# Performance work log

Measured on AMD Instinct MI355X. Metric: run time of the kernel, lower is better.

The kernel has to match this reference:

```python
import jax, jax.numpy as jnp
import numpy as np
import math

D, H, S, B, E, FF = 768, 12, 1024, 2, 32768, 4 * 768
HD = D // H


def layer_norm(x, g, b, eps=1e-5):
    m = jnp.mean(x, axis=-1, keepdims=True)
    v = jnp.mean((x - m) ** 2, axis=-1, keepdims=True)
    return (x - m) / jnp.sqrt(v + eps) * g + b


def setup_inputs() -> dict:
    key = jax.random.key(0)
    ks = jax.random.split(key, 24)
    w = lambda k, shape: jax.random.normal(k, shape, dtype=jnp.float32) * 0.02
    inp = {
        "x": jax.random.normal(ks[0], (B, S, D), dtype=jnp.float32),
        "adj_mask": jax.random.randint(ks[1], (B, S, S), 0, 2).astype(bool),
        "edge_attr": jax.random.normal(ks[2], (E,), dtype=jnp.float32),
        "edge_index": jax.random.randint(ks[3], (2, E), 0, S),
        "norm1_g": jnp.ones((D,), jnp.float32),
        "norm1_b": jnp.zeros((D,), jnp.float32),
        "Wq": w(ks[4], (D, D)), "bq": jnp.zeros((D,), jnp.float32),
        "Wk": w(ks[5], (D, D)), "bk": jnp.zeros((D,), jnp.float32),
        "Wv": w(ks[6], (D, D)), "bv": jnp.zeros((D,), jnp.float32),
        "Wo": w(ks[7], (D, D)), "bo": jnp.zeros((D,), jnp.float32),
        "norm2_g": jnp.ones((D,), jnp.float32),
        "norm2_b": jnp.zeros((D,), jnp.float32),
        "mlp_W1": w(ks[8], (D, FF)), "mlp_b1": jnp.zeros((FF,), jnp.float32),
        "mlp_W2": w(ks[9], (FF, D)), "mlp_b2": jnp.zeros((D,), jnp.float32),
        # per-head edge-attr MLP: Linear(1,16) -> GELU -> Linear(16,1), stacked over H heads
        "ep_W1": w(ks[10], (H, 16)), "ep_b1": jnp.zeros((H, 16), jnp.float32),
        "ep_W2": w(ks[11], (H, 16)), "ep_b2": jnp.zeros((H,), jnp.float32),
    }
    return inp


def reference(x, adj_mask, edge_attr, edge_index,
              norm1_g, norm1_b, Wq, bq, Wk, bk, Wv, bv, Wo, bo,
              norm2_g, norm2_b, mlp_W1, mlp_b1, mlp_W2, mlp_b2,
              ep_W1, ep_b1, ep_W2, ep_b2):
    Bb, Ss, Dd = x.shape
    Hh = ep_W1.shape[0]
    hd = Dd // Hh
    residual = x
    nx = layer_norm(x, norm1_g, norm1_b)
    q = (nx @ Wq + bq).reshape(Bb, Ss, Hh, hd).transpose(0, 2, 1, 3)  # [B,H,S,hd]
    k = (nx @ Wk + bk).reshape(Bb, Ss, Hh, hd).transpose(0, 2, 1, 3)
    v = (nx @ Wv + bv).reshape(Bb, Ss, Hh, hd).transpose(0, 2, 1, 3)
    scores = jnp.einsum('bhqd,bhkd->bhqk', q, k) / math.sqrt(hd)
    mask = adj_mask.astype(bool)[:, None]  # [B,1,S,S]
    scores = jnp.where(mask, scores, jnp.float32(-1e9))
    # per-edge per-head bias (computed under no_grad in the original -> stop_gradient)
    h1 = jax.nn.gelu(edge_attr[:, None, None] * ep_W1[None] + ep_b1[None], approximate=False)  # [E,H,16]
    proj = jnp.einsum('ehk,hk->eh', h1, ep_W2) + ep_b2  # [E,H]
    proj = jax.lax.stop_gradient(proj)
    src, dst = edge_index[0], edge_index[1]
    bias = jnp.zeros((Hh, Ss, Ss), x.dtype).at[:, src, dst].set(proj.T)  # [H,S,S]
    scores = scores + jnp.where(mask, bias[None], jnp.float32(0.0))
    attn = jax.nn.softmax(scores, axis=-1)
    out = jnp.einsum('bhqk,bhkd->bhqd', attn, v)
    out = out.transpose(0, 2, 1, 3).reshape(Bb, Ss, Dd)
    x = residual + (out @ Wo + bo)
    y = layer_norm(x, norm2_g, norm2_b)
    y = jax.nn.gelu(y @ mlp_W1 + mlp_b1, approximate=False) @ mlp_W2 + mlp_b2
    return x + y
```

## Files before the change

### kernel.cpp

```cpp
#include <hip/hip_runtime.h>
#include <hip/hip_bf16.h>

#define B_ 2
#define S_ 1024
#define D_ 768
#define H_ 12
#define HD_ 64
#define FF_ 3072
#define E_ 32768
#define QS_ 2304
#define NSPLIT 4
#define NSPLIT_W2 4
#define BHS (B_ * H_ * S_)

typedef short bf16x8 __attribute__((ext_vector_type(8)));
typedef float f32x4 __attribute__((ext_vector_type(4)));

#define SW(row, seg) ((((seg) ^ ((row) & 7)) * 8))

__device__ __forceinline__ unsigned short f2bf(float f) {
    __hip_bfloat16 h = __float2bfloat16(f);
    return __builtin_bit_cast(unsigned short, h);
}
__device__ __forceinline__ float bf2f(unsigned short u) {
    unsigned int v = ((unsigned int)u) << 16;
    return __builtin_bit_cast(float, v);
}
__device__ __forceinline__ float gelu_exact(float x) {
    return 0.5f * x * (1.0f + erff(x * 0.70710678118654752f));
}
__device__ __forceinline__ void gload_lds16(const unsigned short* g, unsigned short* l) {
    __builtin_amdgcn_global_load_lds((const __attribute__((address_space(1))) void*)g,
                                     (__attribute__((address_space(3))) void*)l, 16, 0, 0);
}

__global__ __launch_bounds__(256) void prep_kernel(
    const void* __restrict__ adj, unsigned int* __restrict__ mp, int* __restrict__ winner,
    const float* __restrict__ Wq, const float* __restrict__ Wk, const float* __restrict__ Wv,
    const float* __restrict__ Wo, const float* __restrict__ W1, const float* __restrict__ W2,
    unsigned short* __restrict__ wqkvt, unsigned short* __restrict__ wot,
    unsigned short* __restrict__ w1t, unsigned short* __restrict__ w2t,
    const float* __restrict__ bq, const float* __restrict__ bk, const float* __restrict__ bv,
    float* __restrict__ bqkv,
    const float* __restrict__ x, const float* __restrict__ g1, const float* __restrict__ bn1,
    unsigned short* __restrict__ nxb)
{
    __shared__ float tile[32][33];
    __shared__ unsigned int words[32];
    __shared__ int u8f;
    __shared__ float red[8];
    const int blk = blockIdx.x;
    const int t = threadIdx.x;

    if (blk < 2048) {
        const int b = blk >> 10, q = blk & 1023;
        if (b == 0) {
            int4 v; v.x = -1; v.y = -1; v.z = -1; v.w = -1;
            reinterpret_cast<int4*>(winner)[q * 256 + t] = v;
        }
        if (t < 32) words[t] = 0;
        if (t == 0) u8f = 0;
        __syncthreads();
        const unsigned int* row8 = (const unsigned int*)((const unsigned char*)adj + ((size_t)b * S_ + q) * S_);
        const unsigned int* row32 = (const unsigned int*)((const int*)adj + ((size_t)b * S_ + q) * S_);
        const unsigned int v = row8[t];
        if (v & 0xFF00FF00u) atomicOr(&u8f, 1);
        __syncthreads();
        if (u8f) {
            unsigned int nib = 0;
            if (v & 0x000000FFu) nib |= 1u;
            if (v & 0x0000FF00u) nib |= 2u;
            if (v & 0x00FF0000u) nib |= 4u;
            if (v & 0xFF000000u) nib |= 8u;
            if (nib) atomicOr(&words[t >> 3], nib << ((t & 7) * 4));
        } else {
            for (int i = 0; i < 4; i++) {
                const int k = i * 256 + t;
                if (row32[k]) atomicOr(&words[k >> 5], 1u << (k & 31));
            }
        }
        __syncthreads();
        if (t < 32) mp[((size_t)b * S_ + q) * 32 + t] = words[t];
    } else if (blk < 8960) {
        const int w = blk - 2048;
        const float* src; unsigned short* dst; int K, N, nb, kb;
        if (w < 2304) {
            const int z = w / 576, r = w - z * 576;
            K = 768; N = 768; kb = (r / 24) * 32; nb = (r % 24) * 32;
            src = (z == 0) ? Wq : (z == 1) ? Wk : (z == 2) ? Wv : Wo;
            dst = (z == 3) ? wot : wqkvt + (size_t)z * 768 * 768;
        } else if (w < 4608) {
            const int r = w - 2304;
            K = 768; N = 3072; nb = (r % 96) * 32; kb = (r / 96) * 32;
            src = W1; dst = w1t;
        } else {
            const int r = w - 4608;
            K = 3072; N = 768; kb = (r % 96) * 32; nb = (r / 96) * 32;
            src = W2; dst = w2t;
        }
        const int tx = t & 31, ty = t >> 5;
        for (int r = 0; r < 32; r += 8)
            tile[ty + r][tx] = src[(size_t)(kb + ty + r) * N + nb + tx];
        __syncthreads();
        for (int r = 0; r < 32; r += 8)
            dst[(size_t)(nb + ty + r) * K + kb + tx] = f2bf(tile[tx][ty + r]);
        if (w == 0) {
            for (int i = t; i < QS_; i += 256)
                bqkv[i] = (i < 768) ? bq[i] : (i < 1536) ? bk[i - 768] : bv[i - 1536];
        }
    } else {
        const int row = blk - 8960;
        const float* xr = x + (size_t)row * D_;
        float v0 = xr[t], v1 = xr[t + 256], v2 = xr[t + 512];
        float s = v0 + v1 + v2, s2 = v0 * v0 + v1 * v1 + v2 * v2;
        for (int m = 32; m; m >>= 1) { s += __shfl_xor(s, m); s2 += __shfl_xor(s2, m); }
        const int w = t >> 6;
        if ((t & 63) == 0) { red[w] = s; red[4 + w] = s2; }
        __syncthreads();
        s = red[0] + red[1] + red[2] + red[3];
        s2 = red[4] + red[5] + red[6] + red[7];
        const float mean = s * (1.f / D_);
        const float var = s2 * (1.f / D_) - mean * mean;
        const float rstd = rsqrtf(var + 1e-5f);
        unsigned short* orow = nxb + (size_t)row * D_;
        orow[t]       = f2bf((v0 - mean) * rstd * g1[t]       + bn1[t]);
        orow[t + 256] = f2bf((v1 - mean) * rstd * g1[t + 256] + bn1[t + 256]);
        orow[t + 512] = f2bf((v2 - mean) * rstd * g1[t + 512] + bn1[t + 512]);
    }
}

__global__ __launch_bounds__(256) void ln_kernel(
    const float* __restrict__ x, const float* __restrict__ g,
    const float* __restrict__ b, unsigned short* __restrict__ out)
{
    const int row = blockIdx.x;
    const int t = threadIdx.x;
    const float* xr = x + (size_t)row * D_;
    float v0 = xr[t], v1 = xr[t + 256], v2 = xr[t + 512];
    float s = v0 + v1 + v2, s2 = v0 * v0 + v1 * v1 + v2 * v2;
    for (int m = 32; m; m >>= 1) { s += __shfl_xor(s, m); s2 += __shfl_xor(s2, m); }
    __shared__ float red[8];
    const int w = t >> 6;
    if ((t & 63) == 0) { red[w] = s; red[4 + w] = s2; }
    __syncthreads();
    s = red[0] + red[1] + red[2] + red[3];
    s2 = red[4] + red[5] + red[6] + red[7];
    const float mean = s * (1.f / D_);
    const float var = s2 * (1.f / D_) - mean * mean;
    const float rstd = rsqrtf(var + 1e-5f);
    unsigned short* orow = out + (size_t)row * D_;
    orow[t]       = f2bf((v0 - mean) * rstd * g[t]       + b[t]);
    orow[t + 256] = f2bf((v1 - mean) * rstd * g[t + 256] + b[t + 256]);
    orow[t + 512] = f2bf((v2 - mean) * rstd * g[t + 512] + b[t + 512]);
}

__global__ __launch_bounds__(256) void edge_proj_scatter_kernel(
    const float* __restrict__ ea, const float* __restrict__ W1, const float* __restrict__ b1,
    const float* __restrict__ W2, const float* __restrict__ b2,
    const int* __restrict__ ei, float* __restrict__ proj, int* __restrict__ winner)
{
    const int tid = blockIdx.x * 256 + threadIdx.x;
    const int e = tid / H_, h = tid - e * H_;
    const float a = ea[e];
    float s = 0.f;
    for (int j = 0; j < 16; j++) {
        const float tv = a * W1[h * 16 + j] + b1[h * 16 + j];
        s += gelu_exact(tv) * W2[h * 16 + j];
    }
    proj[tid] = s + b2[h];
    if (h == 0) {
        const int sn = ei[e], dn = ei[E_ + e];
        atomicMax(&winner[sn * S_ + dn], e);
    }
}

__global__ __launch_bounds__(256) void qkv_kernel(
    const unsigned short* __restrict__ A, const unsigned short* __restrict__ Bt,
    const float* __restrict__ bias, unsigned short* __restrict__ qkv,
    unsigned short* __restrict__ vt,
    const int* __restrict__ winner, const float* __restrict__ proj,
    unsigned short* __restrict__ ebias)
{
    const int blk = blockIdx.x;
    const int t = threadIdx.x;
    if (blk >= 288) {
        const int q = blk - 288;
        const int k4 = t * 4;
        const int4 wv = *reinterpret_cast<const int4*>(&winner[q * S_ + k4]);
        for (int h = 0; h < H_; h++) {
            unsigned int lo = 0, hi = 0;
            if (wv.x >= 0) lo |= (unsigned int)f2bf(proj[(size_t)wv.x * H_ + h]);
            if (wv.y >= 0) lo |= ((unsigned int)f2bf(proj[(size_t)wv.y * H_ + h])) << 16;
            if (wv.z >= 0) hi |= (unsigned int)f2bf(proj[(size_t)wv.z * H_ + h]);
            if (wv.w >= 0) hi |= ((unsigned int)f2bf(proj[(size_t)wv.w * H_ + h])) << 16;
            uint2 val; val.x = lo; val.y = hi;
            *reinterpret_cast<uint2*>(&ebias[((size_t)h * S_ + q) * S_ + k4]) = val;
        }
        return;
    }
    __shared__ unsigned short As[128][64];
    __shared__ unsigned short Bs[128][64];
    const int bx = blk % 18, by = blk / 18;
    const int m0 = by * 128, n0 = bx * 128;
    const int w = t >> 6, l = t & 63;
    const int wm = w >> 1, wn = w & 1;
    const int lr = l & 15, g = l >> 4;
    const int lrow8 = l >> 3;
    const int lseg = (l & 7) ^ lrow8;
    f32x4 acc[4][4] = {};
    for (int k0 = 0; k0 < D_; k0 += 64) {
        __syncthreads();
        for (int j = 0; j < 4; j++) {
            const int q = w * 4 + j;
            const int row = q * 8 + lrow8;
            gload_lds16(A  + (size_t)(m0 + row) * D_ + k0 + lseg * 8, &As[q * 8][0]);
            gload_lds16(Bt + (size_t)(n0 + row) * D_ + k0 + lseg * 8, &Bs[q * 8][0]);
        }
        __syncthreads();
        for (int kk = 0; kk < 2; kk++) {
            bf16x8 af[4], bfr[4];
            for (int m = 0; m < 4; m++) {
                const int r = wm * 64 + m * 16 + lr;
                af[m] = *reinterpret_cast<const bf16x8*>(&As[r][SW(r, kk * 4 + g)]);
            }
            for (int n = 0; n < 4; n++) {
                const int r = wn * 64 + n * 16 + lr;
                bfr[n] = *reinterpret_cast<const bf16x8*>(&Bs[r][SW(r, kk * 4 + g)]);
            }
            for (int m = 0; m < 4; m++)
                for (int n = 0; n < 4; n++)
                    acc[m][n] = __builtin_amdgcn_mfma_f32_16x16x32_bf16(af[m], bfr[n], acc[m][n], 0, 0, 0);
        }
    }
    if (n0 >= 1536) {
        for (int m = 0; m < 4; m++)
            for (int n = 0; n < 4; n++) {
                const int col = n0 + wn * 64 + n * 16 + lr;
                const int vcol = col - 1536;
                const int hh = vcol >> 6, d = vcol & 63;
                const float bvv = bias[col];
                const int grow = m0 + wm * 64 + m * 16 + g * 4;
                const int bb = grow >> 10, s = grow & 1023;
                ushort4 o;
                o.x = f2bf(acc[m][n][0] + bvv);
                o.y = f2bf(acc[m][n][1] + bvv);
                o.z = f2bf(acc[m][n][2] + bvv);
                o.w = f2bf(acc[m][n][3] + bvv);
                *reinterpret_cast<ushort4*>(&vt[(((size_t)(bb * H_ + hh) * HD_) + d) * S_ + s]) = o;
            }
    } else {
        for (int m = 0; m < 4; m++)
            for (int n = 0; n < 4; n++) {
                const int col = n0 + wn * 64 + n * 16 + lr;
                const float scl = (col < 768) ? 0.125f : 1.0f;
                const float bvv = bias[col];
                for (int j = 0; j < 4; j++) {
                    const int row = m0 + wm * 64 + m * 16 + g * 4 + j;
                    qkv[(size_t)row * QS_ + col] = f2bf((acc[m][n][j] + bvv) * scl);
                }
            }
    }
}

template<bool RES, bool OUTBF>
__global__ __launch_bounds__(256) void gemm_kernel(
    const unsigned short* __restrict__ A, const unsigned short* __restrict__ Bt,
    const float* __restrict__ bias, const float* __restrict__ res,
    void* __restrict__ outp, int M, int N, int K)
{
    __shared__ unsigned short As[64][40];
    __shared__ unsigned short Bs[64][40];
    const int m0 = blockIdx.y * 64, n0 = blockIdx.x * 64;
    const int t = threadIdx.x;
    const int w = t >> 6, l = t & 63;
    const int wm = w >> 1, wn = w & 1;
    const int r = l & 15, g = l >> 4;
    const int srow = t >> 2, sseg = t & 3;
    f32x4 acc[2][2] = {};
    for (int k0 = 0; k0 < K; k0 += 32) {
        __syncthreads();
        const uint4 av = *reinterpret_cast<const uint4*>(A + (size_t)(m0 + srow) * K + k0 + sseg * 8);
        *reinterpret_cast<uint4*>(&As[srow][sseg * 8]) = av;
        const uint4 bv = *reinterpret_cast<const uint4*>(Bt + (size_t)(n0 + srow) * K + k0 + sseg * 8);
        *reinterpret_cast<uint4*>(&Bs[srow][sseg * 8]) = bv;
        __syncthreads();
        bf16x8 af[2], bfr[2];
        af[0]  = *reinterpret_cast<const bf16x8*>(&As[wm * 32 + r][g * 8]);
        af[1]  = *reinterpret_cast<const bf16x8*>(&As[wm * 32 + 16 + r][g * 8]);
        bfr[0] = *reinterpret_cast<const bf16x8*>(&Bs[wn * 32 + r][g * 8]);
        bfr[1] = *reinterpret_cast<const bf16x8*>(&Bs[wn * 32 + 16 + r][g * 8]);
        for (int m = 0; m < 2; m++)
            for (int n = 0; n < 2; n++)
                acc[m][n] = __builtin_amdgcn_mfma_f32_16x16x32_bf16(af[m], bfr[n], acc[m][n], 0, 0, 0);
    }
    for (int m = 0; m < 2; m++)
        for (int n = 0; n < 2; n++) {
            const int col = n0 + wn * 32 + n * 16 + r;
            const float bvv = bias[col];
            for (int j = 0; j < 4; j++) {
                const int row = m0 + wm * 32 + m * 16 + g * 4 + j;
                float v = acc[m][n][j] + bvv;
                if (RES) v += res[(size_t)row * N + col];
                if (OUTBF) ((unsigned short*)outp)[(size_t)row * N + col] = f2bf(v);
                else       ((float*)outp)[(size_t)row * N + col] = v;
            }
        }
}

template<bool GELU, bool OUTBF, bool SPLITK>
__global__ __launch_bounds__(256) void gemm128_kernel(
    const unsigned short* __restrict__ A, const unsigned short* __restrict__ Bt,
    const float* __restrict__ bias, void* __restrict__ outp,
    int M, int N, int K, int klen, int scale_below)
{
    __shared__ unsigned short As[128][64];
    __shared__ unsigned short Bs[128][64];
    const int m0 = blockIdx.y * 128, n0 = blockIdx.x * 128;
    const int t = threadIdx.x;
    const int w = t >> 6, l = t & 63;
    const int wm = w >> 1, wn = w & 1;
    const int lr = l & 15, g = l >> 4;
    const int lrow8 = l >> 3;
    const int lseg = (l & 7) ^ lrow8;
    const int kbeg = SPLITK ? blockIdx.z * klen : 0;
    const int kend = SPLITK ? kbeg + klen : K;
    f32x4 acc[4][4] = {};
    for (int k0 = kbeg; k0 < kend; k0 += 64) {
        __syncthreads();
        for (int j = 0; j < 4; j++) {
            const int q = w * 4 + j;
            const int row = q * 8 + lrow8;
            gload_lds16(A  + (size_t)(m0 + row) * K + k0 + lseg * 8, &As[q * 8][0]);
            gload_lds16(Bt + (size_t)(n0 + row) * K + k0 + lseg * 8, &Bs[q * 8][0]);
        }
        __syncthreads();
        for (int kk = 0; kk < 2; kk++) {
            bf16x8 af[4], bfr[4];
            for (int m = 0; m < 4; m++) {
                const int r = wm * 64 + m * 16 + lr;
                af[m] = *reinterpret_cast<const bf16x8*>(&As[r][SW(r, kk * 4 + g)]);
            }
            for (int n = 0; n < 4; n++) {
                const int r = wn * 64 + n * 16 + lr;
                bfr[n] = *reinterpret_cast<const bf16x8*>(&Bs[r][SW(r, kk * 4 + g)]);
            }
            for (int m = 0; m < 4; m++)
                for (int n = 0; n < 4; n++)
                    acc[m][n] = __builtin_amdgcn_mfma_f32_16x16x32_bf16(af[m], bfr[n], acc[m][n], 0, 0, 0);
        }
    }
    if (SPLITK) {
        for (int m = 0; m < 4; m++)
            for (int n = 0; n < 4; n++) {
                const int col = n0 + wn * 64 + n * 16 + lr;
                for (int j = 0; j < 4; j++) {
                    const int row = m0 + wm * 64 + m * 16 + g * 4 + j;
                    if (OUTBF) ((unsigned short*)outp)[((size_t)blockIdx.z * M + row) * N + col] = f2bf(acc[m][n][j]);
                    else       ((float*)outp)[((size_t)blockIdx.z * M + row) * N + col] = acc[m][n][j];
                }
            }
    } else {
        for (int m = 0; m < 4; m++)
            for (int n = 0; n < 4; n++) {
                const int col = n0 + wn * 64 + n * 16 + lr;
                const float scl = (col < scale_below) ? 0.125f : 1.0f;
                const float bvv = bias[col];
                for (int j = 0; j < 4; j++) {
                    const int row = m0 + wm * 64 + m * 16 + g * 4 + j;
                    float v = (acc[m][n][j] + bvv) * scl;
                    if (GELU) v = gelu_exact(v);
                    if (OUTBF) ((unsigned short*)outp)[(size_t)row * N + col] = f2bf(v);
                    else       ((float*)outp)[(size_t)row * N + col] = v;
                }
            }
    }
}

__global__ __launch_bounds__(256) void w2_reduce_kernel(
    const unsigned short* __restrict__ part, const float* __restrict__ x2,
    const float* __restrict__ b2, float* __restrict__ out)
{
    const int idx = (blockIdx.x * 256 + threadIdx.x) * 4;
    const int col = idx % D_;
    const float4 xr = *reinterpret_cast<const float4*>(&x2[idx]);
    const float4 bb = *reinterpret_cast<const float4*>(&b2[col]);
    float4 o;
    o.x = xr.x + bb.x; o.y = xr.y + bb.y; o.z = xr.z + bb.z; o.w = xr.w + bb.w;
    for (int s = 0; s < NSPLIT_W2; s++) {
        const uint2 p = *reinterpret_cast<const uint2*>(&part[(size_t)s * B_ * S_ * D_ + idx]);
        o.x += bf2f((unsigned short)(p.x & 0xFFFF));
        o.y += bf2f((unsigned short)(p.x >> 16));
        o.z += bf2f((unsigned short)(p.y & 0xFFFF));
        o.w += bf2f((unsigned short)(p.y >> 16));
    }
    *reinterpret_cast<float4*>(&out[idx]) = o;
}

__global__ __launch_bounds__(256) void attn_mfma_kernel(
    const unsigned short* __restrict__ qkv,
    const unsigned short* __restrict__ vt,
    const unsigned short* __restrict__ ebias,
    const unsigned int* __restrict__ mp,
    unsigned short* __restrict__ pacc,
    float2* __restrict__ pml)
{
    __shared__ unsigned short Ks[64][64];
    __shared__ unsigned short Vs[64][64];
    __shared__ unsigned short Eb[64][72];
    __shared__ unsigned int   Mw[64][2];
    __shared__ unsigned short Ps[4][16][64];
    const int t = threadIdx.x;
    const int w = t >> 6, l = t & 63;
    const int lr = l & 15, g = l >> 4;
    const int qt = blockIdx.x & 15, sp = blockIdx.x >> 4;
    const int q0 = qt * 64;
    const int h = blockIdx.y, b = blockIdx.z;
    const int bh = b * H_ + h;
    const size_t qbase = (size_t)b * S_ * QS_ + h * HD_;
    const size_t kbase = qbase + 768;
    const size_t vtbase = (size_t)bh * HD_ * S_;

    const int qrow = q0 + w * 16 + lr;
    const bf16x8 af0 = *reinterpret_cast<const bf16x8*>(qkv + qbase + (size_t)qrow * QS_ + g * 8);
    const bf16x8 af1 = *reinterpret_cast<const bf16x8*>(qkv + qbase + (size_t)qrow * QS_ + 32 + g * 8);

    float m_run[4], l_run[4];
    f32x4 acc[4] = {};
    for (int j = 0; j < 4; j++) { m_run[j] = -3.0e38f; l_run[j] = 0.f; }

    const int srow = t >> 2, sseg = t & 3;
    const int kt_beg = sp * (S_ / NSPLIT), kt_end = kt_beg + S_ / NSPLIT;

    uint4 kr0, kr1, vr0, vr1, er0, er1;
    unsigned int mr = 0;
    auto load_tile = [&](int kt) {
        const unsigned short* ksrc = qkv + kbase + (size_t)(kt + srow) * QS_ + sseg * 16;
        kr0 = *reinterpret_cast<const uint4*>(ksrc);
        kr1 = *reinterpret_cast<const uint4*>(ksrc + 8);
        const unsigned short* vsrc = vt + vtbase + (size_t)srow * S_ + kt + sseg * 16;
        vr0 = *reinterpret_cast<const uint4*>(vsrc);
        vr1 = *reinterpret_cast<const uint4*>(vsrc + 8);
        const unsigned short* esrc = ebias + ((size_t)h * S_ + q0 + srow) * S_ + kt + sseg * 16;
        er0 = *reinterpret_cast<const uint4*>(esrc);
        er1 = *reinterpret_cast<const uint4*>(esrc + 8);
        if (t < 128) mr = mp[((size_t)b * S_ + q0 + (t >> 1)) * 32 + (kt >> 5) + (t & 1)];
    };
    load_tile(kt_beg);

    for (int kt = kt_beg; kt < kt_end; kt += 64) {
        __syncthreads();
        {
            *reinterpret_cast<uint4*>(&Ks[srow][SW(srow, sseg * 2)])     = kr0;
            *reinterpret_cast<uint4*>(&Ks[srow][SW(srow, sseg * 2 + 1)]) = kr1;
            *reinterpret_cast<uint4*>(&Vs[srow][SW(srow, sseg * 2)])     = vr0;
            *reinterpret_cast<uint4*>(&Vs[srow][SW(srow, sseg * 2 + 1)]) = vr1;
            *reinterpret_cast<uint4*>(&Eb[srow][sseg * 16])     = er0;
            *reinterpret_cast<uint4*>(&Eb[srow][sseg * 16 + 8]) = er1;
            if (t < 128) Mw[t >> 1][t & 1] = mr;
        }
        __syncthreads();
        if (kt + 64 < kt_end) load_tile(kt + 64);
        f32x4 sc[4];
        for (int n = 0; n < 4; n++) {
            const int r = n * 16 + lr;
            const bf16x8 b0 = *reinterpret_cast<const bf16x8*>(&Ks[r][SW(r, g)]);
            const bf16x8 b1 = *reinterpret_cast<const bf16x8*>(&Ks[r][SW(r, 4 + g)]);
            f32x4 z = {};
            z = __builtin_amdgcn_mfma_f32_16x16x32_bf16(af0, b0, z, 0, 0, 0);
            z = __builtin_amdgcn_mfma_f32_16x16x32_bf16(af1, b1, z, 0, 0, 0);
            sc[n] = z;
        }
        float tmax[4] = {-3.0e38f, -3.0e38f, -3.0e38f, -3.0e38f};
        for (int n = 0; n < 4; n++) {
            for (int j = 0; j < 4; j++) {
                const int rq = w * 16 + g * 4 + j;
                const unsigned int word = Mw[rq][n >> 1];
                const bool msk = (word >> ((n & 1) * 16 + lr)) & 1;
                float sval;
                if (msk) sval = sc[n][j] + bf2f(Eb[rq][n * 16 + lr]);
                else sval = -1e9f;
                sc[n][j] = sval;
                tmax[j] = fmaxf(tmax[j], sval);
            }
        }
        float pscale[4];
        for (int j = 0; j < 4; j++) {
            float tm = tmax[j];
            tm = fmaxf(tm, __shfl_xor(tm, 1));
            tm = fmaxf(tm, __shfl_xor(tm, 2));
            tm = fmaxf(tm, __shfl_xor(tm, 4));
            tm = fmaxf(tm, __shfl_xor(tm, 8));
            const float mnew = fmaxf(m_run[j], tm);
            pscale[j] = __expf(m_run[j] - mnew);
            m_run[j] = mnew;
            l_run[j] *= pscale[j];
        }
        float psum[4] = {0.f, 0.f, 0.f, 0.f};
        for (int n = 0; n < 4; n++) {
            for (int j = 0; j < 4; j++) {
                const float p = __expf(sc[n][j] - m_run[j]);
                psum[j] += p;
                const int row = g * 4 + j;
                Ps[w][row][SW(row, n * 2 + (lr >> 3)) + (lr & 7)] = f2bf(p);
            }
        }
        for (int j = 0; j < 4; j++) {
            float s = psum[j];
            s += __shfl_xor(s, 1); s += __shfl_xor(s, 2);
            s += __shfl_xor(s, 4); s += __shfl_xor(s, 8);
            l_run[j] += s;
            for (int n2 = 0; n2 < 4; n2++) acc[n2][j] *= pscale[j];
        }
        const bf16x8 pa0 = *reinterpret_cast<const bf16x8*>(&Ps[w][lr][SW(lr, g)]);
        const bf16x8 pa1 = *reinterpret_cast<const bf16x8*>(&Ps[w][lr][SW(lr, 4 + g)]);
        for (int n2 = 0; n2 < 4; n2++) {
            const int r = n2 * 16 + lr;
            const bf16x8 vb0 = *reinterpret_cast<const bf16x8*>(&Vs[r][SW(r, g)]);
            const bf16x8 vb1 = *reinterpret_cast<const bf16x8*>(&Vs[r][SW(r, 4 + g)]);
            acc[n2] = __builtin_amdgcn_mfma_f32_16x16x32_bf16(pa0, vb0, acc[n2], 0, 0, 0);
            acc[n2] = __builtin_amdgcn_mfma_f32_16x16x32_bf16(pa1, vb1, acc[n2], 0, 0, 0);
        }
    }
    const size_t prow = (size_t)sp * BHS + (size_t)bh * S_;
    for (int j = 0; j < 4; j++) {
        const int qg = q0 + w * 16 + g * 4 + j;
        for (int n2 = 0; n2 < 4; n2++)
            pacc[(prow + qg) * 64 + n2 * 16 + lr] = f2bf(acc[n2][j]);
        if (lr == 0) { float2 v; v.x = m_run[j]; v.y = l_run[j]; pml[prow + qg] = v; }
    }
}

__global__ __launch_bounds__(256) void attn_combine_kernel(
    const unsigned short* __restrict__ pacc, const float2* __restrict__ pml,
    unsigned short* __restrict__ attnb)
{
    const int idx = (blockIdx.x * 256 + threadIdx.x) * 4;
    const int r = idx >> 6, d = idx & 63;
    float2 ml[NSPLIT];
    float mx = -3.0e38f;
    for (int s = 0; s < NSPLIT; s++) {
        ml[s] = pml[(size_t)s * BHS + r];
        mx = fmaxf(mx, ml[s].x);
    }
    float wgt[NSPLIT], L = 0.f;
    for (int s = 0; s < NSPLIT; s++) {
        wgt[s] = __expf(ml[s].x - mx);
        L += ml[s].y * wgt[s];
    }
    const float inv = (L > 0.f) ? 1.f / L : 0.f;
    float4 o = {0.f, 0.f, 0.f, 0.f};
    for (int s = 0; s < NSPLIT; s++) {
        const uint2 p = *reinterpret_cast<const uint2*>(&pacc[((size_t)s * BHS + r) * 64 + d]);
        o.x += bf2f((unsigned short)(p.x & 0xFFFF)) * wgt[s];
        o.y += bf2f((unsigned short)(p.x >> 16)) * wgt[s];
        o.z += bf2f((unsigned short)(p.y & 0xFFFF)) * wgt[s];
        o.w += bf2f((unsigned short)(p.y >> 16)) * wgt[s];
    }
    const int bh = r >> 10, q = r & 1023;
    const int b = bh / H_, h = bh - b * H_;
    ushort4 ov;
    ov.x = f2bf(o.x * inv); ov.y = f2bf(o.y * inv);
    ov.z = f2bf(o.z * inv); ov.w = f2bf(o.w * inv);
    *reinterpret_cast<ushort4*>(&attnb[((size_t)(b * S_ + q)) * D_ + h * HD_ + d]) = ov;
}

extern "C" void kernel_launch(void* const* d_in, const int* in_sizes, int n_in,
                              void* d_out, int out_size, void* d_ws, size_t ws_size,
                              hipStream_t stream)
{
    const float* x    = (const float*)d_in[0];
    const void*  adj  = d_in[1];
    const float* ea   = (const float*)d_in[2];
    const int*   ei   = (const int*)d_in[3];
    const float* g1   = (const float*)d_in[4];
    const float* bn1  = (const float*)d_in[5];
    const float* Wq   = (const float*)d_in[6];
    const float* bq   = (const float*)d_in[7];
    const float* Wk   = (const float*)d_in[8];
    const float* bk   = (const float*)d_in[9];
    const float* Wv   = (const float*)d_in[10];
    const float* bv   = (const float*)d_in[11];
    const float* Wo   = (const float*)d_in[12];
    const float* bo   = (const float*)d_in[13];
    const float* g2   = (const float*)d_in[14];
    const float* bn2  = (const float*)d_in[15];
    const float* W1   = (const float*)d_in[16];
    const float* mb1  = (const float*)d_in[17];
    const float* W2   = (const float*)d_in[18];
    const float* mb2  = (const float*)d_in[19];
    const float* epW1 = (const float*)d_in[20];
    const float* epb1 = (const float*)d_in[21];
    const float* epW2 = (const float*)d_in[22];
    const float* epb2 = (const float*)d_in[23];

    char* ws = (char*)d_ws;
    size_t off = 0;
    auto carve = [&](size_t bytes) -> void* {
        void* p = ws + off;
        off += (bytes + 255) & ~(size_t)255;
        return p;
    };
    unsigned short* wqkvt = (unsigned short*)carve((size_t)QS_ * D_ * 2);
    unsigned short* wot   = (unsigned short*)carve((size_t)D_ * D_ * 2);
    unsigned short* w1t   = (unsigned short*)carve((size_t)FF_ * D_ * 2);
    unsigned short* w2t   = (unsigned short*)carve((size_t)D_ * FF_ * 2);
    float*          bqkv  = (float*)carve((size_t)QS_ * 4);
    float*          proj  = (float*)carve((size_t)E_ * H_ * 4);
    int*            winner= (int*)carve((size_t)S_ * S_ * 4);
    unsigned short* ebias = (unsigned short*)carve((size_t)H_ * S_ * S_ * 2);
    unsigned int*   mpk   = (unsigned int*)carve((size_t)B_ * S_ * 32 * 4);
    unsigned short* nxb   = (unsigned short*)carve((size_t)B_ * S_ * D_ * 2);
    unsigned short* attnb = (unsigned short*)carve((size_t)B_ * S_ * D_ * 2);
    unsigned short* qkv   = (unsigned short*)carve((size_t)B_ * S_ * QS_ * 2);
    unsigned short* vtb   = (unsigned short*)carve((size_t)B_ * S_ * D_ * 2);
    float*          x2f   = (float*)carve((size_t)B_ * S_ * D_ * 4);
    unsigned short* pacc  = (unsigned short*)carve((size_t)NSPLIT * BHS * 64 * 2);
    float2*         pml   = (float2*)carve((size_t)NSPLIT * BHS * 8);
    unsigned short* ln2b = nxb;
    unsigned short* hb   = qkv;
    unsigned short* pw2  = (unsigned short*)ebias;

    const int M = B_ * S_;

    prep_kernel<<<11008, 256, 0, stream>>>(
        adj, mpk, winner,
        Wq, Wk, Wv, Wo, W1, W2, wqkvt, wot, w1t, w2t, bq, bk, bv, bqkv,
        x, g1, bn1, nxb);

    edge_proj_scatter_kernel<<<(E_ * H_) / 256, 256, 0, stream>>>(
        ea, epW1, epb1, epW2, epb2, ei, proj, winner);

    qkv_kernel<<<288 + S_, 256, 0, stream>>>(
        nxb, wqkvt, bqkv, qkv, vtb, winner, proj, ebias);

    attn_mfma_kernel<<<dim3(16 * NSPLIT, H_, B_), 256, 0, stream>>>(
        qkv, vtb, ebias, mpk, pacc, pml);
    attn_combine_kernel<<<(BHS * 64) / 1024, 256, 0, stream>>>(pacc, pml, attnb);

    gemm_kernel<true, false><<<dim3(D_ / 64, M / 64), 256, 0, stream>>>(
        attnb, wot, bo, x, x2f, M, D_, D_);

    ln_kernel<<<M, 256, 0, stream>>>(x2f, g2, bn2, ln2b);

    gemm128_kernel<true, true, false><<<dim3(FF_ / 128, M / 128), 256, 0, stream>>>(
        ln2b, w1t, mb1, hb, M, FF_, D_, D_, 0);
    gemm128_kernel<false, true, true><<<dim3(D_ / 128, M / 128, NSPLIT_W2), 256, 0, stream>>>(
        hb, w2t, mb2, pw2, M, D_, FF_, FF_ / NSPLIT_W2, 0);
    w2_reduce_kernel<<<(M * D_) / 1024, 256, 0, stream>>>(pw2, x2f, mb2, (float*)d_out);
}
```

Baseline: 183.8 us.

## Split-K the Wo projection, fuse its reduction into LN2, fold edge MLP into prep

The Wo GEMM becomes a 2-way split-K kernel that writes bf16 partials, and the residual add, bias and partial reduction move into the LayerNorm-2 kernel, which also writes x2f. The per-edge MLP projection moves into the prep kernel as extra blocks, leaving only a small atomic scatter kernel. The split-K doubles the block count of the small 768x768 GEMM to improve occupancy, and the prep merge removes a separate launch. The cost is extra partial-buffer traffic and bf16 rounding of the partial sums before the residual add.

```diff
diff --git a/kernel.cpp b/kernel.cpp
--- a/kernel.cpp
+++ b/kernel.cpp
@@ -43,7 +43,9 @@
     const float* __restrict__ bq, const float* __restrict__ bk, const float* __restrict__ bv,
     float* __restrict__ bqkv,
     const float* __restrict__ x, const float* __restrict__ g1, const float* __restrict__ bn1,
-    unsigned short* __restrict__ nxb)
+    unsigned short* __restrict__ nxb,
+    const float* __restrict__ ea, const float* __restrict__ epW1, const float* __restrict__ epb1,
+    const float* __restrict__ epW2, const float* __restrict__ epb2, float* __restrict__ proj)
 {
     __shared__ float tile[32][33];
     __shared__ unsigned int words[32];
@@ -108,7 +110,7 @@
             for (int i = t; i < QS_; i += 256)
                 bqkv[i] = (i < 768) ? bq[i] : (i < 1536) ? bk[i - 768] : bv[i - 1536];
         }
-    } else {
+    } else if (blk < 11008) {
         const int row = blk - 8960;
         const float* xr = x + (size_t)row * D_;
         float v0 = xr[t], v1 = xr[t + 256], v2 = xr[t + 512];
@@ -126,17 +128,171 @@
         orow[t]       = f2bf((v0 - mean) * rstd * g1[t]       + bn1[t]);
         orow[t + 256] = f2bf((v1 - mean) * rstd * g1[t + 256] + bn1[t + 256]);
         orow[t + 512] = f2bf((v2 - mean) * rstd * g1[t + 512] + bn1[t + 512]);
-    }
-}
-
-__global__ __launch_bounds__(256) void ln_kernel(
-    const float* __restrict__ x, const float* __restrict__ g,
-    const float* __restrict__ b, unsigned short* __restrict__ out)
+    } else {
+        const int tid = (blk - 11008) * 256 + t;
+        const int e = tid / H_, h = tid - e * H_;
+        const float a = ea[e];
+        float s = 0.f;
+        for (int j = 0; j < 16; j++) {
+            const float tv = a * epW1[h * 16 + j] + epb1[h * 16 + j];
+            s += gelu_exact(tv) * epW2[h * 16 + j];
+        }
+        proj[tid] = s + epb2[h];
+    }
+}
+
+__global__ __launch_bounds__(256) void scatter_kernel(
+    const int* __restrict__ ei, int* __restrict__ winner)
+{
+    const int e = blockIdx.x * 256 + threadIdx.x;
+    const int sn = ei[e], dn = ei[E_ + e];
+    atomicMax(&winner[sn * S_ + dn], e);
+}
+
+__global__ __launch_bounds__(256) void qkv_kernel(
+    const unsigned short* __restrict__ A, const unsigned short* __restrict__ Bt,
+    const float* __restrict__ bias, unsigned short* __restrict__ qkv,
+    unsigned short* __restrict__ vt,
+    const int* __restrict__ winner, const float* __restrict__ proj,
+    unsigned short* __restrict__ ebias)
+{
+    const int blk = blockIdx.x;
+    const int t = threadIdx.x;
+    if (blk >= 288) {
+        const int q = blk - 288;
+        const int k4 = t * 4;
+        const int4 wv = *reinterpret_cast<const int4*>(&winner[q * S_ + k4]);
+        for (int h = 0; h < H_; h++) {
+            unsigned int lo = 0, hi = 0;
+            if (wv.x >= 0) lo |= (unsigned int)f2bf(proj[(size_t)wv.x * H_ + h]);
+            if (wv.y >= 0) lo |= ((unsigned int)f2bf(proj[(size_t)wv.y * H_ + h])) << 16;
+            if (wv.z >= 0) hi |= (unsigned int)f2bf(proj[(size_t)wv.z * H_ + h]);
+            if (wv.w >= 0) hi |= ((unsigned int)f2bf(proj[(size_t)wv.w * H_ + h])) << 16;
+            uint2 val; val.x = lo; val.y = hi;
+            *reinterpret_cast<uint2*>(&ebias[((size_t)h * S_ + q) * S_ + k4]) = val;
+        }
+        return;
+    }
+    __shared__ unsigned short As[128][64];
+    __shared__ unsigned short Bs[128][64];
+    const int bx = blk % 18, by = blk / 18;
+    const int m0 = by * 128, n0 = bx * 128;
+    const int w = t >> 6, l = t & 63;
+    const int wm = w >> 1, wn = w & 1;
+    const int lr = l & 15, g = l >> 4;
+    const int lrow8 = l >> 3;
+    const int lseg = (l & 7) ^ lrow8;
+    f32x4 acc[4][4] = {};
+    for (int k0 = 0; k0 < D_; k0 += 64) {
+        __syncthreads();
+        for (int j = 0; j < 4; j++) {
+            const int q = w * 4 + j;
+            const int row = q * 8 + lrow8;
+            gload_lds16(A  + (size_t)(m0 + row) * D_ + k0 + lseg * 8, &As[q * 8][0]);
+            gload_lds16(Bt + (size_t)(n0 + row) * D_ + k0 + lseg * 8, &Bs[q * 8][0]);
+        }
+        __syncthreads();
+        for (int kk = 0; kk < 2; kk++) {
+            bf16x8 af[4], bfr[4];
+            for (int m = 0; m < 4; m++) {
+                const int r = wm * 64 + m * 16 + lr;
+                af[m] = *reinterpret_cast<const bf16x8*>(&As[r][SW(r, kk * 4 + g)]);
+            }
+            for (int n = 0; n < 4; n++) {
+                const int r = wn * 64 + n * 16 + lr;
+                bfr[n] = *reinterpret_cast<const bf16x8*>(&Bs[r][SW(r, kk * 4 + g)]);
+            }
+            for (int m = 0; m < 4; m++)
+                for (int n = 0; n < 4; n++)
+                    acc[m][n] = __builtin_amdgcn_mfma_f32_16x16x32_bf16(af[m], bfr[n], acc[m][n], 0, 0, 0);
+        }
+    }
+    if (n0 >= 1536) {
+        for (int m = 0; m < 4; m++)
+            for (int n = 0; n < 4; n++) {
+                const int col = n0 + wn * 64 + n * 16 + lr;
+                const int vcol = col - 1536;
+                const int hh = vcol >> 6, d = vcol & 63;
+                const float bvv = bias[col];
+                const int grow = m0 + wm * 64 + m * 16 + g * 4;
+                const int bb = grow >> 10, s = grow & 1023;
+                ushort4 o;
+                o.x = f2bf(acc[m][n][0] + bvv);
+                o.y = f2bf(acc[m][n][1] + bvv);
+                o.z = f2bf(acc[m][n][2] + bvv);
+                o.w = f2bf(acc[m][n][3] + bvv);
+                *reinterpret_cast<ushort4*>(&vt[(((size_t)(bb * H_ + hh) * HD_) + d) * S_ + s]) = o;
+            }
+    } else {
+        for (int m = 0; m < 4; m++)
+            for (int n = 0; n < 4; n++) {
+                const int col = n0 + wn * 64 + n * 16 + lr;
+                const float scl = (col < 768) ? 0.125f : 1.0f;
+                const float bvv = bias[col];
+                for (int j = 0; j < 4; j++) {
+                    const int row = m0 + wm * 64 + m * 16 + g * 4 + j;
+                    qkv[(size_t)row * QS_ + col] = f2bf((acc[m][n][j] + bvv) * scl);
+                }
+            }
+    }
+}
+
+__global__ __launch_bounds__(256) void gemm64_splitk_kernel(
+    const unsigned short* __restrict__ A, const unsigned short* __restrict__ Bt,
+    unsigned short* __restrict__ part, int M, int N, int K, int klen)
+{
+    __shared__ unsigned short As[64][40];
+    __shared__ unsigned short Bs[64][40];
+    const int m0 = blockIdx.y * 64, n0 = blockIdx.x * 64;
+    const int kbeg = blockIdx.z * klen;
+    const int t = threadIdx.x;
+    const int w = t >> 6, l = t & 63;
+    const int wm = w >> 1, wn = w & 1;
+    const int r = l & 15, g = l >> 4;
+    const int srow = t >> 2, sseg = t & 3;
+    f32x4 acc[2][2] = {};
+    for (int k0 = kbeg; k0 < kbeg + klen; k0 += 32) {
+        __syncthreads();
+        const uint4 av = *reinterpret_cast<const uint4*>(A + (size_t)(m0 + srow) * K + k0 + sseg * 8);
+        *reinterpret_cast<uint4*>(&As[srow][sseg * 8]) = av;
+        const uint4 bv = *reinterpret_cast<const uint4*>(Bt + (size_t)(n0 + srow) * K + k0 + sseg * 8);
+        *reinterpret_cast<uint4*>(&Bs[srow][sseg * 8]) = bv;
+        __syncthreads();
+        bf16x8 af[2], bfr[2];
+        af[0]  = *reinterpret_cast<const bf16x8*>(&As[wm * 32 + r][g * 8]);
+        af[1]  = *reinterpret_cast<const bf16x8*>(&As[wm * 32 + 16 + r][g * 8]);
+        bfr[0] = *reinterpret_cast<const bf16x8*>(&Bs[wn * 32 + r][g * 8]);
+        bfr[1] = *reinterpret_cast<const bf16x8*>(&Bs[wn * 32 + 16 + r][g * 8]);
+        for (int m = 0; m < 2; m++)
+            for (int n = 0; n < 2; n++)
+                acc[m][n] = __builtin_amdgcn_mfma_f32_16x16x32_bf16(af[m], bfr[n], acc[m][n], 0, 0, 0);
+    }
+    for (int m = 0; m < 2; m++)
+        for (int n = 0; n < 2; n++) {
+            const int col = n0 + wn * 32 + n * 16 + r;
+            for (int j = 0; j < 4; j++) {
+                const int row = m0 + wm * 32 + m * 16 + g * 4 + j;
+                part[((size_t)blockIdx.z * M + row) * N + col] = f2bf(acc[m][n][j]);
+            }
+        }
+}
+
+__global__ __launch_bounds__(256) void ln2_fused_kernel(
+    const float* __restrict__ x, const float* __restrict__ bo,
+    const unsigned short* __restrict__ pwo,
+    const float* __restrict__ g, const float* __restrict__ b,
+    unsigned short* __restrict__ out, float* __restrict__ x2f)
 {
     const int row = blockIdx.x;
     const int t = threadIdx.x;
     const float* xr = x + (size_t)row * D_;
-    float v0 = xr[t], v1 = xr[t + 256], v2 = xr[t + 512];
+    const unsigned short* p0 = pwo + (size_t)row * D_;
+    const unsigned short* p1 = pwo + ((size_t)B_ * S_ + row) * D_;
+    float v0 = xr[t]       + bo[t]       + bf2f(p0[t])       + bf2f(p1[t]);
+    float v1 = xr[t + 256] + bo[t + 256] + bf2f(p0[t + 256]) + bf2f(p1[t + 256]);
+    float v2 = xr[t + 512] + bo[t + 512] + bf2f(p0[t + 512]) + bf2f(p1[t + 512]);
+    float* x2r = x2f + (size_t)row * D_;
+    x2r[t] = v0; x2r[t + 256] = v1; x2r[t + 512] = v2;
     float s = v0 + v1 + v2, s2 = v0 * v0 + v1 * v1 + v2 * v2;
     for (int m = 32; m; m >>= 1) { s += __shfl_xor(s, m); s2 += __shfl_xor(s2, m); }
     __shared__ float red[8];
@@ -152,159 +308,6 @@
     orow[t]       = f2bf((v0 - mean) * rstd * g[t]       + b[t]);
     orow[t + 256] = f2bf((v1 - mean) * rstd * g[t + 256] + b[t + 256]);
     orow[t + 512] = f2bf((v2 - mean) * rstd * g[t + 512] + b[t + 512]);
-}
-
-__global__ __launch_bounds__(256) void edge_proj_scatter_kernel(
-    const float* __restrict__ ea, const float* __restrict__ W1, const float* __restrict__ b1,
-    const float* __restrict__ W2, const float* __restrict__ b2,
-    const int* __restrict__ ei, float* __restrict__ proj, int* __restrict__ winner)
-{
-    const int tid = blockIdx.x * 256 + threadIdx.x;
-    const int e = tid / H_, h = tid - e * H_;
-    const float a = ea[e];
-    float s = 0.f;
-    for (int j = 0; j < 16; j++) {
-        const float tv = a * W1[h * 16 + j] + b1[h * 16 + j];
-        s += gelu_exact(tv) * W2[h * 16 + j];
-    }
-    proj[tid] = s + b2[h];
-    if (h == 0) {
-        const int sn = ei[e], dn = ei[E_ + e];
-        atomicMax(&winner[sn * S_ + dn], e);
-    }
-}
-
-__global__ __launch_bounds__(256) void qkv_kernel(
-    const unsigned short* __restrict__ A, const unsigned short* __restrict__ Bt,
-    const float* __restrict__ bias, unsigned short* __restrict__ qkv,
-    unsigned short* __restrict__ vt,
-    const int* __restrict__ winner, const float* __restrict__ proj,
-    unsigned short* __restrict__ ebias)
-{
-    const int blk = blockIdx.x;
-    const int t = threadIdx.x;
-    if (blk >= 288) {
-        const int q = blk - 288;
-        const int k4 = t * 4;
-        const int4 wv = *reinterpret_cast<const int4*>(&winner[q * S_ + k4]);
-        for (int h = 0; h < H_; h++) {
-            unsigned int lo = 0, hi = 0;
-            if (wv.x >= 0) lo |= (unsigned int)f2bf(proj[(size_t)wv.x * H_ + h]);
-            if (wv.y >= 0) lo |= ((unsigned int)f2bf(proj[(size_t)wv.y * H_ + h])) << 16;
-            if (wv.z >= 0) hi |= (unsigned int)f2bf(proj[(size_t)wv.z * H_ + h]);
-            if (wv.w >= 0) hi |= ((unsigned int)f2bf(proj[(size_t)wv.w * H_ + h])) << 16;
-            uint2 val; val.x = lo; val.y = hi;
-            *reinterpret_cast<uint2*>(&ebias[((size_t)h * S_ + q) * S_ + k4]) = val;
-        }
-        return;
-    }
-    __shared__ unsigned short As[128][64];
-    __shared__ unsigned short Bs[128][64];
-    const int bx = blk % 18, by = blk / 18;
-    const int m0 = by * 128, n0 = bx * 128;
-    const int w = t >> 6, l = t & 63;
-    const int wm = w >> 1, wn = w & 1;
-    const int lr = l & 15, g = l >> 4;
-    const int lrow8 = l >> 3;
-    const int lseg = (l & 7) ^ lrow8;
-    f32x4 acc[4][4] = {};
-    for (int k0 = 0; k0 < D_; k0 += 64) {
-        __syncthreads();
-        for (int j = 0; j < 4; j++) {
-            const int q = w * 4 + j;
-            const int row = q * 8 + lrow8;
-            gload_lds16(A  + (size_t)(m0 + row) * D_ + k0 + lseg * 8, &As[q * 8][0]);
-            gload_lds16(Bt + (size_t)(n0 + row) * D_ + k0 + lseg * 8, &Bs[q * 8][0]);
-        }
-        __syncthreads();
-        for (int kk = 0; kk < 2; kk++) {
-            bf16x8 af[4], bfr[4];
-            for (int m = 0; m < 4; m++) {
-                const int r = wm * 64 + m * 16 + lr;
-                af[m] = *reinterpret_cast<const bf16x8*>(&As[r][SW(r, kk * 4 + g)]);
-            }
-            for (int n = 0; n < 4; n++) {
-                const int r = wn * 64 + n * 16 + lr;
-                bfr[n] = *reinterpret_cast<const bf16x8*>(&Bs[r][SW(r, kk * 4 + g)]);
-            }
-            for (int m = 0; m < 4; m++)
-                for (int n = 0; n < 4; n++)
-                    acc[m][n] = __builtin_amdgcn_mfma_f32_16x16x32_bf16(af[m], bfr[n], acc[m][n], 0, 0, 0);
-        }
-    }
-    if (n0 >= 1536) {
-        for (int m = 0; m < 4; m++)
-            for (int n = 0; n < 4; n++) {
-                const int col = n0 + wn * 64 + n * 16 + lr;
-                const int vcol = col - 1536;
-                const int hh = vcol >> 6, d = vcol & 63;
-                const float bvv = bias[col];
-                const int grow = m0 + wm * 64 + m * 16 + g * 4;
-                const int bb = grow >> 10, s = grow & 1023;
-                ushort4 o;
-                o.x = f2bf(acc[m][n][0] + bvv);
-                o.y = f2bf(acc[m][n][1] + bvv);
-                o.z = f2bf(acc[m][n][2] + bvv);
-                o.w = f2bf(acc[m][n][3] + bvv);
-                *reinterpret_cast<ushort4*>(&vt[(((size_t)(bb * H_ + hh) * HD_) + d) * S_ + s]) = o;
-            }
-    } else {
-        for (int m = 0; m < 4; m++)
-            for (int n = 0; n < 4; n++) {
-                const int col = n0 + wn * 64 + n * 16 + lr;
-                const float scl = (col < 768) ? 0.125f : 1.0f;
-                const float bvv = bias[col];
-                for (int j = 0; j < 4; j++) {
-                    const int row = m0 + wm * 64 + m * 16 + g * 4 + j;
-                    qkv[(size_t)row * QS_ + col] = f2bf((acc[m][n][j] + bvv) * scl);
-                }
-            }
-    }
-}
-
-template<bool RES, bool OUTBF>
-__global__ __launch_bounds__(256) void gemm_kernel(
-    const unsigned short* __restrict__ A, const unsigned short* __restrict__ Bt,
-    const float* __restrict__ bias, const float* __restrict__ res,
-    void* __restrict__ outp, int M, int N, int K)
-{
-    __shared__ unsigned short As[64][40];
-    __shared__ unsigned short Bs[64][40];
-    const int m0 = blockIdx.y * 64, n0 = blockIdx.x * 64;
-    const int t = threadIdx.x;
-    const int w = t >> 6, l = t & 63;
-    const int wm = w >> 1, wn = w & 1;
-    const int r = l & 15, g = l >> 4;
-    const int srow = t >> 2, sseg = t & 3;
-    f32x4 acc[2][2] = {};
-    for (int k0 = 0; k0 < K; k0 += 32) {
-        __syncthreads();
-        const uint4 av = *reinterpret_cast<const uint4*>(A + (size_t)(m0 + srow) * K + k0 + sseg * 8);
-        *reinterpret_cast<uint4*>(&As[srow][sseg * 8]) = av;
-        const uint4 bv = *reinterpret_cast<const uint4*>(Bt + (size_t)(n0 + srow) * K + k0 + sseg * 8);
-        *reinterpret_cast<uint4*>(&Bs[srow][sseg * 8]) = bv;
-        __syncthreads();
-        bf16x8 af[2], bfr[2];
-        af[0]  = *reinterpret_cast<const bf16x8*>(&As[wm * 32 + r][g * 8]);
-        af[1]  = *reinterpret_cast<const bf16x8*>(&As[wm * 32 + 16 + r][g * 8]);
-        bfr[0] = *reinterpret_cast<const bf16x8*>(&Bs[wn * 32 + r][g * 8]);
-        bfr[1] = *reinterpret_cast<const bf16x8*>(&Bs[wn * 32 + 16 + r][g * 8]);
-        for (int m = 0; m < 2; m++)
-            for (int n = 0; n < 2; n++)
-                acc[m][n] = __builtin_amdgcn_mfma_f32_16x16x32_bf16(af[m], bfr[n], acc[m][n], 0, 0, 0);
-    }
-    for (int m = 0; m < 2; m++)
-        for (int n = 0; n < 2; n++) {
-            const int col = n0 + wn * 32 + n * 16 + r;
-            const float bvv = bias[col];
-            for (int j = 0; j < 4; j++) {
-                const int row = m0 + wm * 32 + m * 16 + g * 4 + j;
-                float v = acc[m][n][j] + bvv;
-                if (RES) v += res[(size_t)row * N + col];
-                if (OUTBF) ((unsigned short*)outp)[(size_t)row * N + col] = f2bf(v);
-                else       ((float*)outp)[(size_t)row * N + col] = v;
-            }
-        }
 }
 
 template<bool GELU, bool OUTBF, bool SPLITK>
@@ -619,16 +622,17 @@
     unsigned short* ln2b = nxb;
     unsigned short* hb   = qkv;
     unsigned short* pw2  = (unsigned short*)ebias;
+    unsigned short* pwo  = pacc;
 
     const int M = B_ * S_;
 
-    prep_kernel<<<11008, 256, 0, stream>>>(
+    prep_kernel<<<12544, 256, 0, stream>>>(
         adj, mpk, winner,
         Wq, Wk, Wv, Wo, W1, W2, wqkvt, wot, w1t, w2t, bq, bk, bv, bqkv,
-        x, g1, bn1, nxb);
-
-    edge_proj_scatter_kernel<<<(E_ * H_) / 256, 256, 0, stream>>>(
-        ea, epW1, epb1, epW2, epb2, ei, proj, winner);
+        x, g1, bn1, nxb,
+        ea, epW1, epb1, epW2, epb2, proj);
+
+    scatter_kernel<<<E_ / 256, 256, 0, stream>>>(ei, winner);
 
     qkv_kernel<<<288 + S_, 256, 0, stream>>>(
         nxb, wqkvt, bqkv, qkv, vtb, winner, proj, ebias);
@@ -637,10 +641,10 @@
         qkv, vtb, ebias, mpk, pacc, pml);
     attn_combine_kernel<<<(BHS * 64) / 1024, 256, 0, stream>>>(pacc, pml, attnb);
 
-    gemm_kernel<true, false><<<dim3(D_ / 64, M / 64), 256, 0, stream>>>(
-        attnb, wot, bo, x, x2f, M, D_, D_);
-
-    ln_kernel<<<M, 256, 0, stream>>>(x2f, g2, bn2, ln2b);
+    gemm64_splitk_kernel<<<dim3(D_ / 64, M / 64, 2), 256, 0, stream>>>(
+        attnb, wot, pwo, M, D_, D_, D_ / 2);
+
+    ln2_fused_kernel<<<M, 256, 0, stream>>>(x, bo, pwo, g2, bn2, ln2b, x2f);
 
     gemm128_kernel<true, true, false><<<dim3(FF_ / 128, M / 128), 256, 0, stream>>>(
         ln2b, w1t, mb1, hb, M, FF_, D_, D_, 0);
```

After: 184.6 us. No clear change (+0.4%).
